# Optimization experiments

Measured on AMD Instinct MI355X. Metric: run time of the kernel, lower is better.

The kernel has to match this reference:

```python
import jax, jax.numpy as jnp
import numpy as np

N_FFT = 1024
HOP = 256
WIN = 1024  # win_length == n_fft in ISTFTHead
EPS = 1e-11


def setup_inputs() -> dict:
    key = jax.random.key(0)
    k1, k2 = jax.random.split(key)
    B, T, D = 16, 2048, 512
    x = jax.random.normal(k1, (B, T, D), dtype=jnp.float32)
    W = jax.random.normal(k2, (D, N_FFT + 2), dtype=jnp.float32) * 0.02
    b = jnp.zeros((N_FFT + 2,), dtype=jnp.float32)
    return {"x": x, "W": W, "b": b}


def _istft_head(x, W, b):
    B, T, _ = x.shape
    # Linear projection to n_fft + 2 channels, then (B, 1026, T)
    h = jnp.einsum('btd,do->bto', x, W) + b
    h = jnp.transpose(h, (0, 2, 1))
    mag, p = jnp.split(h, 2, axis=1)          # each (B, 513, T)
    mag = jnp.minimum(jnp.exp(mag), 100.0)    # clip(a_max=100)
    S = mag * (jnp.cos(p) + 1j * jnp.sin(p))  # complex spectrogram
    # irfft along frequency axis -> time-domain frames (B, n_fft, T)
    frames = jnp.fft.irfft(S, n=N_FFT, axis=1, norm='backward')
    window = jnp.hanning(WIN).astype(frames.dtype)
    windowed = frames * window[None, :, None]
    out_size = (T - 1) * HOP + WIN
    # overlap-add via segment_sum (matches original _vectorized_overlap_add)
    idx = (jnp.arange(T)[:, None] * HOP + jnp.arange(WIN)[None, :]).ravel()
    vals = jnp.swapaxes(windowed, 1, 2).reshape(B, -1)
    ola = lambda v: jax.ops.segment_sum(v, idx, num_segments=out_size,
                                        indices_are_sorted=False)
    y = jax.vmap(ola)(vals)                   # (B, out_size)
    # window-squared envelope (identical across batch)
    wsq = jnp.broadcast_to((window ** 2)[None, :], (T, WIN)).ravel()
    env = jax.ops.segment_sum(wsq, idx, num_segments=out_size,
                              indices_are_sorted=False)
    y = y / (env + EPS)
    pad = (WIN - HOP) // 2                    # 'same' padding trim
    return y[:, pad:-pad]


def reference(x, W, b):
    return _istft_head(x, W, b)
```

## Files before the change

### kernel.cpp

```cpp
#include <hip/hip_runtime.h>
#include <hip/hip_bf16.h>
#include <cstdint>
#include <cstddef>

typedef __hip_bfloat16 bf16;
using short8 = __attribute__((ext_vector_type(8))) short;
using f32x4  = __attribute__((ext_vector_type(4))) float;

static constexpr float kTwoPi = 6.283185307179586f;

#define GLDS(g, l) __builtin_amdgcn_global_load_lds(                       \
    (const __attribute__((address_space(1))) uint32_t*)(g),                \
    (__attribute__((address_space(3))) uint32_t*)(l), 16, 0, 0)

#define BAR()   { __builtin_amdgcn_sched_barrier(0); __builtin_amdgcn_s_barrier(); \
                  asm volatile("" ::: "memory"); }
#define LGKM0() { asm volatile("s_waitcnt lgkmcnt(0)" ::: "memory"); __builtin_amdgcn_sched_barrier(0); }
#define VM6()   { asm volatile("s_waitcnt vmcnt(6)"   ::: "memory"); __builtin_amdgcn_sched_barrier(0); }
#define VM0()   { asm volatile("s_waitcnt vmcnt(0)"   ::: "memory"); __builtin_amdgcn_sched_barrier(0); }

static __device__ __forceinline__ float b2f(short u) {
    union { short s; bf16 h; } c; c.s = u; return __bfloat162float(c.h);
}

__global__ void prep_w_k(const float* __restrict__ W, const float* __restrict__ b,
                         bf16* __restrict__ Wr, float* __restrict__ br,
                         float* __restrict__ Wcp) {
    int j = blockIdx.x;
    if (j < 1024) {
        int col = (j & 1) ? 513 + (j >> 1) : (j >> 1);
        for (int k = threadIdx.x; k < 512; k += 256)
            Wr[(size_t)j * 512 + k] = __float2bfloat16(W[(size_t)k * 1026 + col]);
        if (threadIdx.x == 0) br[j] = b[col];
    } else {
        int col = (j == 1024) ? 512 : 1025;
        for (int k = threadIdx.x; k < 512; k += 256)
            Wcp[(j - 1024) * 512 + k] = W[(size_t)k * 1026 + col];
        if (threadIdx.x == 0) Wcp[1024 + (j - 1024)] = b[col];
    }
}

__global__ void cvt_x_k(const float* __restrict__ x, bf16* __restrict__ xb,
                        const float* __restrict__ Wcp, float* __restrict__ R512) {
    const int tid = threadIdx.x, w = tid >> 6, lane = tid & 63;
    size_t i = ((size_t)blockIdx.x * 256 + tid) * 8;
    float4 a = *(const float4*)(x + i);
    float4 c = *(const float4*)(x + i + 4);
    union { bf16 h[8]; uint4 u; } o;
    o.h[0] = __float2bfloat16(a.x); o.h[1] = __float2bfloat16(a.y);
    o.h[2] = __float2bfloat16(a.z); o.h[3] = __float2bfloat16(a.w);
    o.h[4] = __float2bfloat16(c.x); o.h[5] = __float2bfloat16(c.y);
    o.h[6] = __float2bfloat16(c.z); o.h[7] = __float2bfloat16(c.w);
    *(uint4*)(xb + i) = o.u;
    const int kb = lane * 8;
    float4 m0 = *(const float4*)(Wcp + kb);
    float4 m1 = *(const float4*)(Wcp + kb + 4);
    float4 p0 = *(const float4*)(Wcp + 512 + kb);
    float4 p1 = *(const float4*)(Wcp + 512 + kb + 4);
    float dm = a.x*m0.x + a.y*m0.y + a.z*m0.z + a.w*m0.w
             + c.x*m1.x + c.y*m1.y + c.z*m1.z + c.w*m1.w;
    float dp = a.x*p0.x + a.y*p0.y + a.z*p0.z + a.w*p0.w
             + c.x*p1.x + c.y*p1.y + c.z*p1.z + c.w*p1.w;
    #pragma unroll
    for (int off = 32; off; off >>= 1) {
        dm += __shfl_xor(dm, off);
        dp += __shfl_xor(dp, off);
    }
    if (lane == 0) {
        float mag = fminf(__expf(dm + Wcp[1024]), 100.0f);
        R512[blockIdx.x * 4 + w] = mag * __cosf(dp + Wcp[1025]);
    }
}

__global__ void prep_mcs_k(bf16* __restrict__ Mc, bf16* __restrict__ Ms) {
    const int r = blockIdx.x;
    for (int kk = threadIdx.x; kk < 512; kk += 256) {
        float vc = 0.0f, vs = 0.0f;
        if (r <= 512) {
            int mm = (kk * r) & 1023;
            float ang = kTwoPi * (float)mm * (1.0f / 1024.0f);
            float alpha = (kk == 0) ? 1.0f : 2.0f;
            vc = alpha * (1.0f / 1024.0f) * cosf(ang);
            vs = alpha * (1.0f / 1024.0f) * sinf(ang);
        }
        Mc[(size_t)r * 512 + kk] = __float2bfloat16(vc);
        Ms[(size_t)r * 512 + kk] = __float2bfloat16(vs);
    }
}

__global__ void prep_win_k(float* __restrict__ wg) {
    const int idx = blockIdx.x * 256 + threadIdx.x;
    float wn = 0.5f - 0.5f * cosf(kTwoPi * (float)idx / 1023.0f);
    wg[idx] = wn;
    wg[1024 + idx] = wn * wn;
}

__global__ __launch_bounds__(512, 2)
void gemm1_k(const bf16* __restrict__ A, const bf16* __restrict__ B,
             const float* __restrict__ bias, bf16* __restrict__ O)
{
    extern __shared__ __align__(16) bf16 lds[];
    const int tid  = threadIdx.x;
    const int w    = tid >> 6;
    const int lane = tid & 63;
    const int wr = w >> 1, wc = w & 1;

    const int nwg = gridDim.x, orig = blockIdx.x;
    const int bid = (orig & 7) * (nwg >> 3) + (orig >> 3);
    const int nt = bid & 7, mt = bid >> 3;
    const int row0 = mt * 256;
    const int col0 = nt * 128;

    const int srow  = lane >> 3;
    const int sslot = (lane & 7) ^ srow;

    const bf16* gA0 = A + (size_t)(row0 + srow) * 512 + sslot * 8;
    const bf16* gB0 = B + (size_t)(col0 + srow) * 512 + sslot * 8;

    auto stage = [&](int t, int s) {
        bf16* lA = lds + s * 24576;
        bf16* lB = lA + 16384;
        #pragma unroll
        for (int l = 0; l < 4; ++l) {
            const int c = w * 4 + l;
            GLDS(gA0 + (size_t)(8 * c) * 512 + (size_t)t * 64, lA + c * 512 + lane * 8);
        }
        #pragma unroll
        for (int l = 0; l < 2; ++l) {
            const int d = w * 2 + l;
            GLDS(gB0 + (size_t)(8 * d) * 512 + (size_t)t * 64, lB + d * 512 + lane * 8);
        }
    };

    short8 af[4][2], bq[4][2];
    auto ldregs = [&](int s) {
        const bf16* lA = lds + s * 24576;
        const bf16* lB = lA + 16384;
        #pragma unroll
        for (int fm = 0; fm < 4; ++fm)
            #pragma unroll
            for (int ks = 0; ks < 2; ++ks) {
                const int r  = wr * 64 + fm * 16 + (lane & 15);
                const int sl = (ks * 4 + (lane >> 4)) ^ (r & 7);
                af[fm][ks] = *(const short8*)(lA + r * 64 + sl * 8);
            }
        #pragma unroll
        for (int fn = 0; fn < 4; ++fn)
            #pragma unroll
            for (int ks = 0; ks < 2; ++ks) {
                const int r  = wc * 64 + fn * 16 + (lane & 15);
                const int sl = (ks * 4 + (lane >> 4)) ^ (r & 7);
                bq[fn][ks] = *(const short8*)(lB + r * 64 + sl * 8);
            }
    };

    f32x4 acc[4][4] = {};

    stage(0, 0);
    stage(1, 1);
    VM6();
    BAR();

    for (int t = 0; t < 8; ++t) {
        const int tp = (t + 2 < 8) ? t + 2 : 7;
        ldregs(t % 3);
        stage(tp, (t + 2) % 3);
        VM6();
        LGKM0();
        BAR();
        __builtin_amdgcn_s_setprio(1);
        #pragma unroll
        for (int ks = 0; ks < 2; ++ks)
            #pragma unroll
            for (int fm = 0; fm < 4; ++fm)
                #pragma unroll
                for (int fn = 0; fn < 4; ++fn)
                    acc[fm][fn] = __builtin_amdgcn_mfma_f32_16x16x32_bf16(
                        af[fm][ks], bq[fn][ks], acc[fm][fn], 0, 0, 0);
        __builtin_amdgcn_s_setprio(0);
    }
    VM0();
    BAR();

    char* eb = (char*)lds;
    #pragma unroll
    for (int fm = 0; fm < 4; ++fm) {
        #pragma unroll
        for (int fn = 0; fn < 4; ++fn) {
            const int col = wc * 64 + fn * 16 + (lane & 15);
            const int n   = col0 + col;
            #pragma unroll
            for (int r = 0; r < 4; ++r) {
                const int row = wr * 64 + fm * 16 + (lane >> 4) * 4 + r;
                float v = acc[fm][fn][r] + bias[n];
                float vo = __shfl_xor(v, 1);
                float res = (n & 1) ? fminf(__expf(vo), 100.0f) * __sinf(v)
                                    : fminf(__expf(v), 100.0f) * __cosf(vo);
                const int colp = (col >> 1) + ((col & 1) << 6);
                const int sw = (colp >> 3) ^ (((row >> 2) & 7) << 1);
                *(bf16*)(eb + row * 256 + sw * 16 + (colp & 7) * 2) =
                    __float2bfloat16(res);
            }
        }
    }
    asm volatile("s_waitcnt lgkmcnt(0)" ::: "memory");
    BAR();

    #pragma unroll
    for (int k2 = 0; k2 < 8; ++k2) {
        const int g   = tid + k2 * 512;
        const int row = g >> 4;
        const int s   = g & 15;
        const int sw  = s ^ (((row >> 2) & 7) << 1);
        short8 vv = *(const short8*)(eb + row * 256 + sw * 16);
        const int colg = col0 + s * 8;
        *(short8*)(O + (size_t)(row0 + row) * 1032 + colg) = vv;
    }
}

__global__ __launch_bounds__(512, 1)
void gemm2_k(const bf16* __restrict__ S, const bf16* __restrict__ Mc,
             const bf16* __restrict__ Ms, bf16* __restrict__ pe,
             bf16* __restrict__ po)
{
    extern __shared__ __align__(16) bf16 lds[];
    const int tid  = threadIdx.x;
    const int w    = tid >> 6;
    const int lane = tid & 63;
    const int wr = w >> 1, wc = w & 1;

    const int nwg = gridDim.x, orig = blockIdx.x;
    const int bid = (orig & 7) * (nwg >> 3) + (orig >> 3);
    const int nt = bid % 5, mt = bid / 5;
    const int row0 = mt * 256;
    const int col0 = nt * 128;

    const int srow  = lane >> 3;
    const int sslot = (lane & 7) ^ srow;

    const bf16* gA0 = S  + (size_t)(row0 + srow) * 1032 + sslot * 8;
    const bf16* gBc = Mc + (size_t)(col0 + srow) * 512 + sslot * 8;
    const bf16* gBs = Ms + (size_t)(col0 + srow) * 512 + sslot * 8;

    auto stage = [&](int t, int s) {
        bf16* lA = lds + s * 24576;
        bf16* lB = lA + 16384;
        const bf16* gB = (t < 8) ? gBc : gBs;
        const size_t aoff = (t < 8) ? (size_t)t * 128 : (size_t)(t - 8) * 128 + 64;
        const int tk = t & 7;
        #pragma unroll
        for (int l = 0; l < 4; ++l) {
            const int c = w * 4 + l;
            GLDS(gA0 + (size_t)(8 * c) * 1032 + aoff, lA + c * 512 + lane * 8);
        }
        #pragma unroll
        for (int l = 0; l < 2; ++l) {
            const int d = w * 2 + l;
            GLDS(gB + (size_t)(8 * d) * 512 + (size_t)tk * 64, lB + d * 512 + lane * 8);
        }
    };

    short8 af[4][2], bq[4][2];
    auto ldregs = [&](int s) {
        const bf16* lA = lds + s * 24576;
        const bf16* lB = lA + 16384;
        #pragma unroll
        for (int fm = 0; fm < 4; ++fm)
            #pragma unroll
            for (int ks = 0; ks < 2; ++ks) {
                const int r  = wr * 64 + fm * 16 + (lane & 15);
                const int sl = (ks * 4 + (lane >> 4)) ^ (r & 7);
                af[fm][ks] = *(const short8*)(lA + r * 64 + sl * 8);
            }
        #pragma unroll
        for (int fn = 0; fn < 4; ++fn)
            #pragma unroll
            for (int ks = 0; ks < 2; ++ks) {
                const int r  = wc * 64 + fn * 16 + (lane & 15);
                const int sl = (ks * 4 + (lane >> 4)) ^ (r & 7);
                bq[fn][ks] = *(const short8*)(lB + r * 64 + sl * 8);
            }
    };

    f32x4 accE[4][4] = {}, accO[4][4] = {};

    #define MMA2(ACC) {                                                        \
        __builtin_amdgcn_s_setprio(1);                                         \
        _Pragma("unroll") for (int ks = 0; ks < 2; ++ks)                       \
          _Pragma("unroll") for (int fm = 0; fm < 4; ++fm)                     \
            _Pragma("unroll") for (int fn = 0; fn < 4; ++fn)                   \
              ACC[fm][fn] = __builtin_amdgcn_mfma_f32_16x16x32_bf16(           \
                  af[fm][ks], bq[fn][ks], ACC[fm][fn], 0, 0, 0);               \
        __builtin_amdgcn_s_setprio(0); }

    stage(0, 0);
    stage(1, 1);
    VM6();
    BAR();

    for (int t = 0; t < 8; ++t) {
        ldregs(t % 3);
        stage(t + 2, (t + 2) % 3);
        VM6();
        LGKM0();
        BAR();
        MMA2(accE);
    }
    for (int t = 8; t < 16; ++t) {
        const int tp = (t + 2 < 16) ? t + 2 : 15;
        ldregs(t % 3);
        stage(tp, (t + 2) % 3);
        VM6();
        LGKM0();
        BAR();
        MMA2(accO);
    }
    VM0();
    BAR();
    #undef MMA2

    char* eb = (char*)lds;
    #define EPIPASS(ACC, DST) {                                                 \
        _Pragma("unroll") for (int fm = 0; fm < 4; ++fm)                        \
        _Pragma("unroll") for (int fn = 0; fn < 4; ++fn) {                      \
            const int col = wc * 64 + fn * 16 + (lane & 15);                    \
            _Pragma("unroll") for (int r = 0; r < 4; ++r) {                     \
                const int row = wr * 64 + fm * 16 + (lane >> 4) * 4 + r;        \
                const int sw = (col >> 3) ^ (((row >> 2) & 7) << 1);            \
                *(bf16*)(eb + row * 256 + sw * 16 + (col & 7) * 2) =            \
                    __float2bfloat16(ACC[fm][fn][r]);                           \
            }                                                                   \
        }                                                                       \
        asm volatile("s_waitcnt lgkmcnt(0)" ::: "memory");                      \
        BAR();                                                                  \
        _Pragma("unroll") for (int k2 = 0; k2 < 8; ++k2) {                      \
            const int g   = tid + k2 * 512;                                     \
            const int row = g >> 4;                                             \
            const int s   = g & 15;                                             \
            const int sw  = s ^ (((row >> 2) & 7) << 1);                        \
            short8 vv = *(const short8*)(eb + row * 256 + sw * 16);             \
            const int colg = col0 + s * 8;                                      \
            if (colg + 8 <= 520)                                                \
                *(short8*)(DST + (size_t)(row0 + row) * 520 + colg) = vv;       \
        }                                                                       \
        BAR();                                                                  \
    }
    EPIPASS(accE, pe)
    EPIPASS(accO, po)
    #undef EPIPASS
}

__global__ void ola_k(const bf16* __restrict__ pe, const bf16* __restrict__ po,
                      const float* __restrict__ R512, const float* __restrict__ wg,
                      float* __restrict__ out) {
    __shared__ float w[1024], w2[1024];
    for (int i = threadIdx.x; i < 1024; i += 256) { w[i] = wg[i]; w2[i] = wg[1024 + i]; }
    __syncthreads();
    const int gid = blockIdx.x * 256 + threadIdx.x;
    const int o0  = gid * 8;
    const int bb  = o0 >> 19;
    const int oo  = o0 & 524287;
    const int s   = oo + 384;
    const int tmax = s >> 8;
    float sum[8] = {}, env[8] = {};
    #pragma unroll
    for (int jj = 0; jj < 4; ++jj) {
        const int t = tmax - jj;
        if (t < 0 || t >= 2048) continue;
        const int n0 = s - (t << 8);
        const size_t rowi = (size_t)bb * 2048 + t;
        const size_t rb = rowi * 520;
        const float rc = R512[rowi] * (1.0f / 1024.0f);
        if (n0 <= 504) {
            short8 E  = *(const short8*)(pe + rb + n0);
            short8 Og = *(const short8*)(po + rb + n0);
            #pragma unroll
            for (int e = 0; e < 8; ++e) {
                float ev = b2f(E[e]) + ((e & 1) ? -rc : rc);
                sum[e] += (ev - b2f(Og[e])) * w[n0 + e];
                env[e] += w2[n0 + e];
            }
        } else {
            const int nb = 1024 - n0;
            short8 Ea = *(const short8*)(pe + rb + nb - 8);
            short8 Eb = *(const short8*)(pe + rb + nb);
            short8 Oa = *(const short8*)(po + rb + nb - 8);
            short8 Ob = *(const short8*)(po + rb + nb);
            sum[0] += (b2f(Eb[0]) + rc + b2f(Ob[0])) * w[n0];
            env[0] += w2[n0];
            #pragma unroll
            for (int j = 1; j < 8; ++j) {
                float ev = b2f(Ea[8 - j]) + ((j & 1) ? -rc : rc);
                sum[j] += (ev + b2f(Oa[8 - j])) * w[n0 + j];
                env[j] += w2[n0 + j];
            }
        }
    }
    float4 r0, r1;
    r0.x = sum[0] / (env[0] + 1e-11f); r0.y = sum[1] / (env[1] + 1e-11f);
    r0.z = sum[2] / (env[2] + 1e-11f); r0.w = sum[3] / (env[3] + 1e-11f);
    r1.x = sum[4] / (env[4] + 1e-11f); r1.y = sum[5] / (env[5] + 1e-11f);
    r1.z = sum[6] / (env[6] + 1e-11f); r1.w = sum[7] / (env[7] + 1e-11f);
    *(float4*)(out + o0)     = r0;
    *(float4*)(out + o0 + 4) = r1;
}

extern "C" void kernel_launch(void* const* d_in, const int* in_sizes, int n_in,
                              void* d_out, int out_size, void* d_ws, size_t ws_size,
                              hipStream_t stream)
{
    const float* x = (const float*)d_in[0];
    const float* W = (const float*)d_in[1];
    const float* b = (const float*)d_in[2];
    float* out = (float*)d_out;

    char* ws = (char*)d_ws;
    size_t off = 0;
    auto alloc = [&](size_t bytes) { char* p = ws + off; off += (bytes + 255) & ~255ull; return p; };

    bf16*  Mc   = (bf16*) alloc(640ull * 512 * 2);
    bf16*  Ms   = (bf16*) alloc(640ull * 512 * 2);
    float* wg   = (float*)alloc(2048 * 4);
    float* br   = (float*)alloc(1152 * 4);
    float* Wcp  = (float*)alloc(1026 * 4);
    float* R512 = (float*)alloc(32768ull * 4);
    bf16*  Sri  = (bf16*) alloc(32768ull * 1032 * 2);
    char*  regC = alloc(68157440ull);
    bf16*  xb = (bf16*)regC;
    bf16*  Wr = (bf16*)(regC + 33554432ull);
    bf16*  pe = (bf16*)regC;
    bf16*  po = (bf16*)(regC + 34078720ull);

    hipFuncSetAttribute(reinterpret_cast<const void*>(gemm1_k),
                        hipFuncAttributeMaxDynamicSharedMemorySize, 147456);
    hipFuncSetAttribute(reinterpret_cast<const void*>(gemm2_k),
                        hipFuncAttributeMaxDynamicSharedMemorySize, 147456);

    prep_w_k  <<<dim3(1026),  dim3(256), 0, stream>>>(W, b, Wr, br, Wcp);
    cvt_x_k   <<<dim3(8192),  dim3(256), 0, stream>>>(x, xb, Wcp, R512);
    prep_mcs_k<<<dim3(640),   dim3(256), 0, stream>>>(Mc, Ms);
    prep_win_k<<<dim3(4),     dim3(256), 0, stream>>>(wg);
    gemm1_k<<<dim3(1024), dim3(512), 147456, stream>>>(xb, Wr, br, Sri);
    gemm2_k<<<dim3(640), dim3(512), 147456, stream>>>(Sri, Mc, Ms, pe, po);
    ola_k  <<<dim3(4096), dim3(256), 0, stream>>>(pe, po, R512, wg, out);
    (void)in_sizes; (void)n_in; (void)out_size; (void)ws_size;
}
```

Measured before the change: 183.3 us.

## Halve K-tile depth to shrink LDS and split gemm2 even/odd across blocks

Both GEMMs now stage 32-wide K slices instead of 64, with a new XOR swizzle for the narrower rows. This halves the LDS footprint to 72KB and the per-wave fragment registers, so launch bounds can ask for 4 blocks per CU. gemm2 no longer accumulates the even and odd (cos/sin) outputs in one block; they go to separate blocks, doubling the grid to 1280 and halving the accumulators each block holds. The aim is more occupancy and parallelism to hide latency, at the cost of more barriers per K, and of A tiles being reloaded by two blocks in gemm2.

```diff
diff --git a/kernel.cpp b/kernel.cpp
--- a/kernel.cpp
+++ b/kernel.cpp
@@ -16,7 +16,7 @@
 #define BAR()   { __builtin_amdgcn_sched_barrier(0); __builtin_amdgcn_s_barrier(); \
                   asm volatile("" ::: "memory"); }
 #define LGKM0() { asm volatile("s_waitcnt lgkmcnt(0)" ::: "memory"); __builtin_amdgcn_sched_barrier(0); }
-#define VM6()   { asm volatile("s_waitcnt vmcnt(6)"   ::: "memory"); __builtin_amdgcn_sched_barrier(0); }
+#define VM3()   { asm volatile("s_waitcnt vmcnt(3)"   ::: "memory"); __builtin_amdgcn_sched_barrier(0); }
 #define VM0()   { asm volatile("s_waitcnt vmcnt(0)"   ::: "memory"); __builtin_amdgcn_sched_barrier(0); }
 
 static __device__ __forceinline__ float b2f(short u) {
@@ -95,7 +95,7 @@
     wg[1024 + idx] = wn * wn;
 }
 
-__global__ __launch_bounds__(512, 2)
+__global__ __launch_bounds__(512, 4)
 void gemm1_k(const bf16* __restrict__ A, const bf16* __restrict__ B,
              const float* __restrict__ bias, bf16* __restrict__ O)
 {
@@ -111,72 +111,61 @@
     const int row0 = mt * 256;
     const int col0 = nt * 128;
 
-    const int srow  = lane >> 3;
-    const int sslot = (lane & 7) ^ srow;
-
-    const bf16* gA0 = A + (size_t)(row0 + srow) * 512 + sslot * 8;
-    const bf16* gB0 = B + (size_t)(col0 + srow) * 512 + sslot * 8;
+    const int q = lane >> 2;
+    const int gslot = (lane & 3) ^ ((lane >> 2) & 3) ^ ((lane >> 4) & 3);
+
+    const bf16* gA0 = A + (size_t)(row0 + q) * 512 + gslot * 8;
+    const bf16* gB0 = B + (size_t)(col0 + q) * 512 + gslot * 8;
 
     auto stage = [&](int t, int s) {
-        bf16* lA = lds + s * 24576;
-        bf16* lB = lA + 16384;
-        #pragma unroll
-        for (int l = 0; l < 4; ++l) {
-            const int c = w * 4 + l;
-            GLDS(gA0 + (size_t)(8 * c) * 512 + (size_t)t * 64, lA + c * 512 + lane * 8);
-        }
+        bf16* lA = lds + s * 12288;
+        bf16* lB = lA + 8192;
         #pragma unroll
         for (int l = 0; l < 2; ++l) {
-            const int d = w * 2 + l;
-            GLDS(gB0 + (size_t)(8 * d) * 512 + (size_t)t * 64, lB + d * 512 + lane * 8);
-        }
+            const int c = w * 2 + l;
+            GLDS(gA0 + (size_t)(16 * c) * 512 + (size_t)t * 32, lA + c * 512 + lane * 8);
+        }
+        GLDS(gB0 + (size_t)(16 * w) * 512 + (size_t)t * 32, lB + w * 512 + lane * 8);
     };
 
-    short8 af[4][2], bq[4][2];
+    short8 af[4], bq[4];
     auto ldregs = [&](int s) {
-        const bf16* lA = lds + s * 24576;
-        const bf16* lB = lA + 16384;
-        #pragma unroll
-        for (int fm = 0; fm < 4; ++fm)
-            #pragma unroll
-            for (int ks = 0; ks < 2; ++ks) {
-                const int r  = wr * 64 + fm * 16 + (lane & 15);
-                const int sl = (ks * 4 + (lane >> 4)) ^ (r & 7);
-                af[fm][ks] = *(const short8*)(lA + r * 64 + sl * 8);
-            }
-        #pragma unroll
-        for (int fn = 0; fn < 4; ++fn)
-            #pragma unroll
-            for (int ks = 0; ks < 2; ++ks) {
-                const int r  = wc * 64 + fn * 16 + (lane & 15);
-                const int sl = (ks * 4 + (lane >> 4)) ^ (r & 7);
-                bq[fn][ks] = *(const short8*)(lB + r * 64 + sl * 8);
-            }
+        const bf16* lA = lds + s * 12288;
+        const bf16* lB = lA + 8192;
+        const int sl = (lane >> 4) ^ (lane & 3) ^ ((lane >> 2) & 3);
+        #pragma unroll
+        for (int fm = 0; fm < 4; ++fm) {
+            const int r = wr * 64 + fm * 16 + (lane & 15);
+            af[fm] = *(const short8*)(lA + r * 32 + sl * 8);
+        }
+        #pragma unroll
+        for (int fn = 0; fn < 4; ++fn) {
+            const int r = wc * 64 + fn * 16 + (lane & 15);
+            bq[fn] = *(const short8*)(lB + r * 32 + sl * 8);
+        }
     };
 
     f32x4 acc[4][4] = {};
 
     stage(0, 0);
     stage(1, 1);
-    VM6();
-    BAR();
-
-    for (int t = 0; t < 8; ++t) {
-        const int tp = (t + 2 < 8) ? t + 2 : 7;
+    VM3();
+    BAR();
+
+    for (int t = 0; t < 16; ++t) {
+        const int tp = (t + 2 < 16) ? t + 2 : 15;
         ldregs(t % 3);
         stage(tp, (t + 2) % 3);
-        VM6();
+        VM3();
         LGKM0();
         BAR();
         __builtin_amdgcn_s_setprio(1);
         #pragma unroll
-        for (int ks = 0; ks < 2; ++ks)
-            #pragma unroll
-            for (int fm = 0; fm < 4; ++fm)
-                #pragma unroll
-                for (int fn = 0; fn < 4; ++fn)
-                    acc[fm][fn] = __builtin_amdgcn_mfma_f32_16x16x32_bf16(
-                        af[fm][ks], bq[fn][ks], acc[fm][fn], 0, 0, 0);
+        for (int fm = 0; fm < 4; ++fm)
+            #pragma unroll
+            for (int fn = 0; fn < 4; ++fn)
+                acc[fm][fn] = __builtin_amdgcn_mfma_f32_16x16x32_bf16(
+                    af[fm], bq[fn], acc[fm][fn], 0, 0, 0);
         __builtin_amdgcn_s_setprio(0);
     }
     VM0();
@@ -218,7 +207,7 @@
     }
 }
 
-__global__ __launch_bounds__(512, 1)
+__global__ __launch_bounds__(512, 4)
 void gemm2_k(const bf16* __restrict__ S, const bf16* __restrict__ Mc,
              const bf16* __restrict__ Ms, bf16* __restrict__ pe,
              bf16* __restrict__ po)
@@ -231,123 +220,103 @@
 
     const int nwg = gridDim.x, orig = blockIdx.x;
     const int bid = (orig & 7) * (nwg >> 3) + (orig >> 3);
-    const int nt = bid % 5, mt = bid / 5;
+    const int eo = (bid >= 640) ? 1 : 0;
+    const int b2 = bid - eo * 640;
+    const int nt = b2 % 5, mt = b2 / 5;
     const int row0 = mt * 256;
     const int col0 = nt * 128;
 
-    const int srow  = lane >> 3;
-    const int sslot = (lane & 7) ^ srow;
-
-    const bf16* gA0 = S  + (size_t)(row0 + srow) * 1032 + sslot * 8;
-    const bf16* gBc = Mc + (size_t)(col0 + srow) * 512 + sslot * 8;
-    const bf16* gBs = Ms + (size_t)(col0 + srow) * 512 + sslot * 8;
+    const int q = lane >> 2;
+    const int gslot = (lane & 3) ^ ((lane >> 2) & 3) ^ ((lane >> 4) & 3);
+
+    const bf16* gA0 = S + (size_t)(row0 + q) * 1032 + (size_t)eo * 64 + gslot * 8;
+    const bf16* gB0 = (eo ? Ms : Mc) + (size_t)(col0 + q) * 512 + gslot * 8;
+    bf16* DST = eo ? po : pe;
 
     auto stage = [&](int t, int s) {
-        bf16* lA = lds + s * 24576;
-        bf16* lB = lA + 16384;
-        const bf16* gB = (t < 8) ? gBc : gBs;
-        const size_t aoff = (t < 8) ? (size_t)t * 128 : (size_t)(t - 8) * 128 + 64;
-        const int tk = t & 7;
-        #pragma unroll
-        for (int l = 0; l < 4; ++l) {
-            const int c = w * 4 + l;
-            GLDS(gA0 + (size_t)(8 * c) * 1032 + aoff, lA + c * 512 + lane * 8);
-        }
+        bf16* lA = lds + s * 12288;
+        bf16* lB = lA + 8192;
+        const size_t aoff = (size_t)(t >> 1) * 128 + (size_t)(t & 1) * 32;
         #pragma unroll
         for (int l = 0; l < 2; ++l) {
-            const int d = w * 2 + l;
-            GLDS(gB + (size_t)(8 * d) * 512 + (size_t)tk * 64, lB + d * 512 + lane * 8);
-        }
+            const int c = w * 2 + l;
+            GLDS(gA0 + (size_t)(16 * c) * 1032 + aoff, lA + c * 512 + lane * 8);
+        }
+        GLDS(gB0 + (size_t)(16 * w) * 512 + (size_t)t * 32, lB + w * 512 + lane * 8);
     };
 
-    short8 af[4][2], bq[4][2];
+    short8 af[4], bq[4];
     auto ldregs = [&](int s) {
-        const bf16* lA = lds + s * 24576;
-        const bf16* lB = lA + 16384;
-        #pragma unroll
-        for (int fm = 0; fm < 4; ++fm)
-            #pragma unroll
-            for (int ks = 0; ks < 2; ++ks) {
-                const int r  = wr * 64 + fm * 16 + (lane & 15);
-                const int sl = (ks * 4 + (lane >> 4)) ^ (r & 7);
-                af[fm][ks] = *(const short8*)(lA + r * 64 + sl * 8);
-            }
-        #pragma unroll
-        for (int fn = 0; fn < 4; ++fn)
-            #pragma unroll
-            for (int ks = 0; ks < 2; ++ks) {
-                const int r  = wc * 64 + fn * 16 + (lane & 15);
-                const int sl = (ks * 4 + (lane >> 4)) ^ (r & 7);
-                bq[fn][ks] = *(const short8*)(lB + r * 64 + sl * 8);
-            }
+        const bf16* lA = lds + s * 12288;
+        const bf16* lB = lA + 8192;
+        const int sl = (lane >> 4) ^ (lane & 3) ^ ((lane >> 2) & 3);
+        #pragma unroll
+        for (int fm = 0; fm < 4; ++fm) {
+            const int r = wr * 64 + fm * 16 + (lane & 15);
+            af[fm] = *(const short8*)(lA + r * 32 + sl * 8);
+        }
+        #pragma unroll
+        for (int fn = 0; fn < 4; ++fn) {
+            const int r = wc * 64 + fn * 16 + (lane & 15);
+            bq[fn] = *(const short8*)(lB + r * 32 + sl * 8);
+        }
     };
 
-    f32x4 accE[4][4] = {}, accO[4][4] = {};
-
-    #define MMA2(ACC) {                                                        \
-        __builtin_amdgcn_s_setprio(1);                                         \
-        _Pragma("unroll") for (int ks = 0; ks < 2; ++ks)                       \
-          _Pragma("unroll") for (int fm = 0; fm < 4; ++fm)                     \
-            _Pragma("unroll") for (int fn = 0; fn < 4; ++fn)                   \
-              ACC[fm][fn] = __builtin_amdgcn_mfma_f32_16x16x32_bf16(           \
-                  af[fm][ks], bq[fn][ks], ACC[fm][fn], 0, 0, 0);               \
-        __builtin_amdgcn_s_setprio(0); }
+    f32x4 acc[4][4] = {};
 
     stage(0, 0);
     stage(1, 1);
-    VM6();
-    BAR();
-
-    for (int t = 0; t < 8; ++t) {
-        ldregs(t % 3);
-        stage(t + 2, (t + 2) % 3);
-        VM6();
-        LGKM0();
-        BAR();
-        MMA2(accE);
-    }
-    for (int t = 8; t < 16; ++t) {
+    VM3();
+    BAR();
+
+    for (int t = 0; t < 16; ++t) {
         const int tp = (t + 2 < 16) ? t + 2 : 15;
         ldregs(t % 3);
         stage(tp, (t + 2) % 3);
-        VM6();
+        VM3();
         LGKM0();
         BAR();
-        MMA2(accO);
+        __builtin_amdgcn_s_setprio(1);
+        #pragma unroll
+        for (int fm = 0; fm < 4; ++fm)
+            #pragma unroll
+            for (int fn = 0; fn < 4; ++fn)
+                acc[fm][fn] = __builtin_amdgcn_mfma_f32_16x16x32_bf16(
+                    af[fm], bq[fn], acc[fm][fn], 0, 0, 0);
+        __builtin_amdgcn_s_setprio(0);
     }
     VM0();
     BAR();
-    #undef MMA2
 
     char* eb = (char*)lds;
-    #define EPIPASS(ACC, DST) {                                                 \
-        _Pragma("unroll") for (int fm = 0; fm < 4; ++fm)                        \
-        _Pragma("unroll") for (int fn = 0; fn < 4; ++fn) {                      \
-            const int col = wc * 64 + fn * 16 + (lane & 15);                    \
-            _Pragma("unroll") for (int r = 0; r < 4; ++r) {                     \
-                const int row = wr * 64 + fm * 16 + (lane >> 4) * 4 + r;        \
-                const int sw = (col >> 3) ^ (((row >> 2) & 7) << 1);            \
-                *(bf16*)(eb + row * 256 + sw * 16 + (col & 7) * 2) =            \
-                    __float2bfloat16(ACC[fm][fn][r]);                           \
-            }                                                                   \
-        }                                                                       \
-        asm volatile("s_waitcnt lgkmcnt(0)" ::: "memory");                      \
-        BAR();                                                                  \
-        _Pragma("unroll") for (int k2 = 0; k2 < 8; ++k2) {                      \
-            const int g   = tid + k2 * 512;                                     \
-            const int row = g >> 4;                                             \
-            const int s   = g & 15;                                             \
-            const int sw  = s ^ (((row >> 2) & 7) << 1);                        \
-            short8 vv = *(const short8*)(eb + row * 256 + sw * 16);             \
-            const int colg = col0 + s * 8;                                      \
-            if (colg + 8 <= 520)                                                \
-                *(short8*)(DST + (size_t)(row0 + row) * 520 + colg) = vv;       \
-        }                                                                       \
-        BAR();                                                                  \
-    }
-    EPIPASS(accE, pe)
-    EPIPASS(accO, po)
-    #undef EPIPASS
+    #pragma unroll
+    for (int fm = 0; fm < 4; ++fm) {
+        #pragma unroll
+        for (int fn = 0; fn < 4; ++fn) {
+            const int col = wc * 64 + fn * 16 + (lane & 15);
+            #pragma unroll
+            for (int r = 0; r < 4; ++r) {
+                const int row = wr * 64 + fm * 16 + (lane >> 4) * 4 + r;
+                const int sw = (col >> 3) ^ (((row >> 2) & 7) << 1);
+                *(bf16*)(eb + row * 256 + sw * 16 + (col & 7) * 2) =
+                    __float2bfloat16(acc[fm][fn][r]);
+            }
+        }
+    }
+    asm volatile("s_waitcnt lgkmcnt(0)" ::: "memory");
+    BAR();
+
+    #pragma unroll
+    for (int k2 = 0; k2 < 8; ++k2) {
+        const int g   = tid + k2 * 512;
+        const int row = g >> 4;
+        const int s   = g & 15;
+        const int sw  = s ^ (((row >> 2) & 7) << 1);
+        short8 vv = *(const short8*)(eb + row * 256 + sw * 16);
+        const int colg = col0 + s * 8;
+        if (colg + 8 <= 520)
+            *(short8*)(DST + (size_t)(row0 + row) * 520 + colg) = vv;
+    }
 }
 
 __global__ void ola_k(const bf16* __restrict__ pe, const bf16* __restrict__ po,
@@ -432,16 +401,16 @@
     bf16*  po = (bf16*)(regC + 34078720ull);
 
     hipFuncSetAttribute(reinterpret_cast<const void*>(gemm1_k),
-                        hipFuncAttributeMaxDynamicSharedMemorySize, 147456);
+                        hipFuncAttributeMaxDynamicSharedMemorySize, 73728);
     hipFuncSetAttribute(reinterpret_cast<const void*>(gemm2_k),
-                        hipFuncAttributeMaxDynamicSharedMemorySize, 147456);
+                        hipFuncAttributeMaxDynamicSharedMemorySize, 73728);
 
     prep_w_k  <<<dim3(1026),  dim3(256), 0, stream>>>(W, b, Wr, br, Wcp);
     cvt_x_k   <<<dim3(8192),  dim3(256), 0, stream>>>(x, xb, Wcp, R512);
     prep_mcs_k<<<dim3(640),   dim3(256), 0, stream>>>(Mc, Ms);
     prep_win_k<<<dim3(4),     dim3(256), 0, stream>>>(wg);
-    gemm1_k<<<dim3(1024), dim3(512), 147456, stream>>>(xb, Wr, br, Sri);
-    gemm2_k<<<dim3(640), dim3(512), 147456, stream>>>(Sri, Mc, Ms, pe, po);
+    gemm1_k<<<dim3(1024), dim3(512), 73728, stream>>>(xb, Wr, br, Sri);
+    gemm2_k<<<dim3(1280), dim3(512), 73728, stream>>>(Sri, Mc, Ms, pe, po);
     ola_k  <<<dim3(4096), dim3(256), 0, stream>>>(pe, po, R512, wg, out);
     (void)in_sizes; (void)n_in; (void)out_size; (void)ws_size;
 }
```

Measured after the change: 171.6 us. -6.4%, faster.
